# Optimization experiments

Measured on AMD Instinct MI355X. Metric: run time of the kernel, lower is better.

Reference implementation:

```python
import jax, jax.numpy as jnp
import numpy as np

INT_MIN = jnp.iinfo(jnp.int32).min


def setup_inputs() -> dict:
    key = jax.random.key(0)
    ks = jax.random.split(key, 12)
    N, E, H, R, T = 200000, 100000, 100, 172, 100
    return {
        'src': jax.random.randint(ks[0], (E,), 0, N, dtype=jnp.int32),
        'dst': jax.random.randint(ks[1], (E,), 0, N, dtype=jnp.int32),
        't': jax.random.randint(ks[2], (E,), 0, 1000000, dtype=jnp.int32),
        'raw_msg': jax.random.normal(ks[3], (E, R), dtype=jnp.float32),
        'memory': jax.random.normal(ks[4], (N, H), dtype=jnp.float32),
        'last_update': jax.random.randint(ks[5], (N,), 0, 1000, dtype=jnp.int32),
        'te_w': jax.random.normal(ks[6], (T, 1), dtype=jnp.float32) * 0.1,
        'te_b': jax.random.normal(ks[7], (T,), dtype=jnp.float32) * 0.1,
        'w_ih': jax.random.normal(ks[8], (3 * H, 2 * H + R + T), dtype=jnp.float32) * 0.05,
        'w_hh': jax.random.normal(ks[9], (3 * H, H), dtype=jnp.float32) * 0.05,
        'b_ih': jax.random.normal(ks[10], (3 * H,), dtype=jnp.float32) * 0.05,
        'b_hh': jax.random.normal(ks[11], (3 * H,), dtype=jnp.float32) * 0.05,
    }


def reference(src, dst, t, raw_msg, memory, last_update, te_w, te_b, w_ih, w_hh, b_ih, b_hh):
    N, H = memory.shape
    E = src.shape[0]

    def time_enc(t_rel):  # Linear(1, time_dim) then cos, t_rel: [E] float
        return jnp.cos(t_rel[:, None] * te_w[:, 0][None, :] + te_b[None, :])

    # IdentityMessage: concat(mem[src], mem[dst], raw_msg, t_enc); two streams (s and d)
    t_enc_s = time_enc((t - last_update[src]).astype(raw_msg.dtype))
    t_enc_d = time_enc((t - last_update[dst]).astype(raw_msg.dtype))
    msg_s = jnp.concatenate([memory[src], memory[dst], raw_msg, t_enc_s], axis=-1)
    msg_d = jnp.concatenate([memory[dst], memory[src], raw_msg, t_enc_d], axis=-1)

    msg = jnp.concatenate([msg_s, msg_d], axis=0)        # [2E, msg_dim]
    idx = jnp.concatenate([src, dst], axis=0)            # [2E]
    t2 = jnp.concatenate([t, t], axis=0)                 # [2E]

    # LastAggregator: per node pick the message with maximum timestamp
    max_t = jnp.full((N,), INT_MIN, dtype=t2.dtype).at[idx].max(t2)
    cand = jnp.where(t2 == max_t[idx], jnp.arange(2 * E, dtype=jnp.int32), jnp.int32(-1))
    win = jnp.full((N,), -1, dtype=jnp.int32).at[idx].max(cand)  # winning edge per node
    has_msg = win >= 0
    aggr = jnp.where(has_msg[:, None], msg[jnp.clip(win, 0)], 0.0)  # [N, msg_dim]

    # GRUCell(msg_dim, H)
    gi = aggr @ w_ih.T + b_ih                             # [N, 3H]
    gh = memory @ w_hh.T + b_hh                           # [N, 3H]
    i_r, i_z, i_n = jnp.split(gi, 3, axis=-1)
    h_r, h_z, h_n = jnp.split(gh, 3, axis=-1)
    r = jax.nn.sigmoid(i_r + h_r)
    z = jax.nn.sigmoid(i_z + h_z)
    n = jnp.tanh(i_n + r * h_n)
    memory_new = (1.0 - z) * n + z * memory               # [N, H]

    last_update_new = last_update.at[idx].max(t2)         # scatter latest event time
    return memory_new, last_update_new
```

## Files before the change

kernel.cpp:

```cpp
#include <hip/hip_runtime.h>
#include <math.h>

typedef __attribute__((ext_vector_type(8))) short  short8;
typedef __attribute__((ext_vector_type(4))) float  f32x4;

static constexpr int H     = 100;
static constexpr int RD    = 172;
static constexpr int WK    = 472;
static constexpr int NKS   = 20;
static constexpr int MB    = 48;
static constexpr int GRPS  = 3;
static constexpr int BLK   = 448;
static constexpr int SLOTS = 64;
static constexpr int NTT   = 28;
static constexpr int BPK_N = NTT * NKS * 64 * 8;

__device__ inline unsigned short f2bf(float x) {
    union { float f; unsigned u; } v; v.f = x;
    return (unsigned short)((v.u + 0x7FFFu + ((v.u >> 16) & 1u)) >> 16);
}
__device__ inline float bf2f(unsigned short b) {
    union { unsigned u; float f; } v; v.u = ((unsigned)b) << 16;
    return v.f;
}
__device__ inline unsigned pkbf(float a, float b) {
    unsigned r;
    asm("v_cvt_pk_bf16_f32 %0, %1, %2" : "=v"(r) : "v"(a), "v"(b));
    return r;
}
__device__ inline f32x4 mfma16(short8 a, short8 b, f32x4 c) {
    return __builtin_amdgcn_mfma_f32_16x16x32_bf16(a, b, c, 0, 0, 0);
}
__device__ inline float4 ld4g(const float* base, int lc, int limit) {
    if (lc + 4 <= limit) return *(const float4*)(base + lc);
    return make_float4(0.f, 0.f, 0.f, 0.f);
}

__global__ __launch_bounds__(256) void k_init(int* __restrict__ maxt, int* __restrict__ win, int N) {
    int i = blockIdx.x * blockDim.x + threadIdx.x;
    if (i < N) { maxt[i] = (int)0x80000000; win[i] = -1; }
}

__global__ __launch_bounds__(256) void k_maxt(const int* __restrict__ src, const int* __restrict__ dst,
                                              const int* __restrict__ t, int* __restrict__ maxt, int E) {
    int j = blockIdx.x * blockDim.x + threadIdx.x;
    if (j < E) {
        int tj = t[j];
        atomicMax(&maxt[src[j]], tj);
        atomicMax(&maxt[dst[j]], tj);
    }
}

__global__ __launch_bounds__(256) void k_win(const int* __restrict__ src, const int* __restrict__ dst,
                                             const int* __restrict__ t, const int* __restrict__ maxt,
                                             int* __restrict__ win, int E) {
    int j = blockIdx.x * blockDim.x + threadIdx.x;
    if (j < E) {
        int tj = t[j];
        int s = src[j], d = dst[j];
        if (maxt[s] == tj) atomicMax(&win[s], j);
        if (maxt[d] == tj) atomicMax(&win[d], j + E);
    }
}

__global__ __launch_bounds__(256) void k_prep(const float* __restrict__ w_ih, const float* __restrict__ w_hh,
                                              unsigned short* __restrict__ B) {
    int idx = blockIdx.x * 256 + threadIdx.x;
    if (idx >= BPK_N) return;
    int jj   = idx & 7;
    int lane = (idx >> 3) & 63;
    int rest = idx >> 9;
    int ks   = rest % NKS;
    int tile = rest / NKS;
    int kk   = ks * 32 + ((lane >> 4) << 3) + jj;
    float v = 0.f;
    if (tile < 21) {
        int gate = tile / 7;
        int tcol = (tile % 7) * 16 + (lane & 15);
        if (tcol < 100) {
            if (kk < 512) {
                int col = -1;
                if (kk < 100)                   col = kk;
                else if (kk >= 104 && kk < 204) col = kk - 4;
                else if (kk >= 208 && kk < 380) col = kk - 8;
                else if (kk >= 384 && kk < 484) col = kk - 12;
                if (col >= 0) v = w_ih[(gate * 100 + tcol) * WK + col];
            } else {
                int khh = kk - 512;
                if (gate < 2 && khh < 100)
                    v = w_hh[(gate * 100 + tcol) * H + khh];
            }
        }
    } else {
        int tcol = (tile - 21) * 16 + (lane & 15);
        int khh  = kk - 512;
        if (tcol < 100 && khh >= 0 && khh < 100)
            v = w_hh[(200 + tcol) * H + khh];
    }
    B[idx] = f2bf(v);
}

__global__ __launch_bounds__(BLK, 4) void k_gru(
    const int* __restrict__ src, const int* __restrict__ dst, const int* __restrict__ t,
    const float* __restrict__ raw_msg, const float* __restrict__ memory,
    const int* __restrict__ last_update, const float* __restrict__ te_w,
    const float* __restrict__ te_b, const float* __restrict__ b_ih,
    const float* __restrict__ b_hh, const int* __restrict__ win,
    const unsigned short* __restrict__ Bpack,
    float* __restrict__ out_mem, float* __restrict__ out_lu, int E, int N)
{
    __shared__ unsigned short sA[GRPS * NKS * SLOTS * 8];
    __shared__ int   s_other[MB];
    __shared__ int   s_j[MB];
    __shared__ int   s_has[MB];
    __shared__ float s_dt[MB];

    const int tid   = threadIdx.x;
    const int node0 = blockIdx.x * MB;

    if (tid < MB) {
        int node = node0 + tid;
        int has = 0, j = 0, other = 0; float dt = 0.f;
        if (node < N) {
            int lu = last_update[node];
            int w  = win[node];
            int te = lu;
            if (w >= 0) {
                has = 1;
                int e = (w < E) ? w : (w - E);
                j = e;
                other = (w < E) ? dst[e] : src[e];
                te = t[e];
                dt = (float)(te - lu);
            }
            out_lu[node] = (float)(te > lu ? te : lu);
        }
        s_j[tid] = j; s_other[tid] = other; s_has[tid] = has; s_dt[tid] = dt;
    }
    __syncthreads();

    if (tid < 432) {
        const int nl    = tid % 48;
        const int c0    = tid / 48;
        const int node  = node0 + nl;
        const bool valid = node < N;
        const int has   = s_has[nl];
        const float* memN = memory + (size_t)node * H;
        const float* memO = memory + (size_t)s_other[nl] * H;
        const float* rawJ = raw_msg + (size_t)s_j[nl] * RD;
        const float dt  = s_dt[nl];
        const int grp = nl >> 4;
        const int row = nl & 15;

        float4 va[8], vb[8];
#pragma unroll
        for (int it = 0; it < 8; ++it) {
            const int cc = c0 + it * 9;
            va[it] = make_float4(0.f, 0.f, 0.f, 0.f); vb[it] = va[it];
            if (cc < 67) {
                const int c  = cc + 13;
                const int kb = c * 8;
                if (c < 64) {
                    if (has) {
                        if (c < 26)      { va[it] = ld4g(memO, kb - 104, 100); vb[it] = ld4g(memO, kb - 100, 100); }
                        else if (c < 48) { va[it] = ld4g(rawJ, kb - 208, RD ); vb[it] = ld4g(rawJ, kb - 204, RD ); }
                        else {
                            const int lc = kb - 384;
                            float vv[8];
#pragma unroll
                            for (int q = 0; q < 8; ++q) {
                                int col = lc + q;
                                vv[q] = (col < 100) ? __cosf(fmaf(dt, te_w[col], te_b[col])) : 0.f;
                            }
                            va[it] = make_float4(vv[0], vv[1], vv[2], vv[3]);
                            vb[it] = make_float4(vv[4], vv[5], vv[6], vv[7]);
                        }
                    }
                } else if (valid) {
                    va[it] = ld4g(memN, kb - 512, 100);
                    vb[it] = ld4g(memN, kb - 508, 100);
                }
            }
        }
#pragma unroll
        for (int it = 0; it < 8; ++it) {
            const int cc = c0 + it * 9;
            if (cc < 67) {
                const int c = cc + 13;
                int4 sv;
                sv.x = (int)pkbf(va[it].x, va[it].y);
                sv.y = (int)pkbf(va[it].z, va[it].w);
                sv.z = (int)pkbf(vb[it].x, vb[it].y);
                sv.w = (int)pkbf(vb[it].z, vb[it].w);
                {
                    const int ks = c >> 2, sub = c & 3;
                    const int slot = sub * 16 + (row ^ (sub << 2));
                    *(int4*)&sA[((grp * NKS + ks) * SLOTS + slot) * 8] = sv;
                }
                if (c >= 64 && c < 77) {
                    int4 sm_;
                    sm_.x = has ? sv.x : 0; sm_.y = has ? sv.y : 0;
                    sm_.z = has ? sv.z : 0; sm_.w = has ? sv.w : 0;
                    const int cm = c - 64;
                    const int ks = cm >> 2, sub = cm & 3;
                    const int slot = sub * 16 + (row ^ (sub << 2));
                    *(int4*)&sA[((grp * NKS + ks) * SLOTS + slot) * 8] = sm_;
                }
            }
        }
    }
    __syncthreads();

    const int wv    = tid >> 6;
    const int lane  = tid & 63;
    const int lrow  = lane & 15;
    const int lhi   = lane >> 4;
    const int slotl = lhi * 16 + (lrow ^ (lhi << 2));

    f32x4 ar[GRPS], az[GRPS], an[GRPS], ah[GRPS];
#pragma unroll
    for (int m = 0; m < GRPS; ++m) { ar[m] = (f32x4)0.f; az[m] = (f32x4)0.f; an[m] = (f32x4)0.f; ah[m] = (f32x4)0.f; }

    __builtin_amdgcn_s_setprio(1);
#pragma unroll
    for (int ks = 0; ks < NKS; ++ks) {
        short8 a0 = *(const short8*)&sA[((0 * NKS + ks) * SLOTS + slotl) * 8];
        short8 a1 = *(const short8*)&sA[((1 * NKS + ks) * SLOTS + slotl) * 8];
        short8 a2 = *(const short8*)&sA[((2 * NKS + ks) * SLOTS + slotl) * 8];
        short8 br = *(const short8*)&Bpack[(((size_t)(     wv) * NKS + ks) * 64 + lane) * 8];
        short8 bz = *(const short8*)&Bpack[(((size_t)( 7 + wv) * NKS + ks) * 64 + lane) * 8];
        short8 bn = (ks < 16)
                  ? *(const short8*)&Bpack[(((size_t)(14 + wv) * NKS + ks) * 64 + lane) * 8]
                  : *(const short8*)&Bpack[(((size_t)(21 + wv) * NKS + ks) * 64 + lane) * 8];
        ar[0] = mfma16(a0, br, ar[0]);  ar[1] = mfma16(a1, br, ar[1]);  ar[2] = mfma16(a2, br, ar[2]);
        az[0] = mfma16(a0, bz, az[0]);  az[1] = mfma16(a1, bz, az[1]);  az[2] = mfma16(a2, bz, az[2]);
        if (ks < 16) { an[0] = mfma16(a0, bn, an[0]);  an[1] = mfma16(a1, bn, an[1]);  an[2] = mfma16(a2, bn, an[2]); }
        else         { ah[0] = mfma16(a0, bn, ah[0]);  ah[1] = mfma16(a1, bn, ah[1]);  ah[2] = mfma16(a2, bn, ah[2]); }
    }
    __builtin_amdgcn_s_setprio(0);

    const int c = wv * 16 + lrow;
    if (c < 100) {
        const float br_ = b_ih[c]       + b_hh[c];
        const float bz_ = b_ih[c + 100] + b_hh[c + 100];
        const float bin = b_ih[c + 200];
        const float bhn = b_hh[c + 200];
        const int ksh = 16 + (c >> 5);
        const int sbh = (c >> 3) & 3;
        const int ceh = c & 7;
#pragma unroll
        for (int m = 0; m < GRPS; ++m) {
#pragma unroll
            for (int r = 0; r < 4; ++r) {
                const int node = node0 + m * 16 + lhi * 4 + r;
                if (node < N) {
                    const int rw   = lhi * 4 + r;
                    const int slot = sbh * 16 + (rw ^ (sbh << 2));
                    const float h  = bf2f(sA[((m * NKS + ksh) * SLOTS + slot) * 8 + ceh]);
                    const float rg = 1.f / (1.f + __expf(-(ar[m][r] + br_)));
                    const float zg = 1.f / (1.f + __expf(-(az[m][r] + bz_)));
                    const float xn = an[m][r] + bin + rg * (ah[m][r] + bhn);
                    const float ex = __expf(2.f * fabsf(xn));
                    const float th = copysignf(1.f - 2.f / (ex + 1.f), xn);
                    out_mem[(size_t)node * H + c] = (1.f - zg) * th + zg * h;
                }
            }
        }
    }
}

extern "C" void kernel_launch(void* const* d_in, const int* in_sizes, int n_in,
                              void* d_out, int out_size, void* d_ws, size_t ws_size,
                              hipStream_t stream)
{
    const int*   src         = (const int*)d_in[0];
    const int*   dst         = (const int*)d_in[1];
    const int*   t           = (const int*)d_in[2];
    const float* raw_msg     = (const float*)d_in[3];
    const float* memory      = (const float*)d_in[4];
    const int*   last_update = (const int*)d_in[5];
    const float* te_w        = (const float*)d_in[6];
    const float* te_b        = (const float*)d_in[7];
    const float* w_ih        = (const float*)d_in[8];
    const float* w_hh        = (const float*)d_in[9];
    const float* b_ih        = (const float*)d_in[10];
    const float* b_hh        = (const float*)d_in[11];

    const int E = in_sizes[0];
    const int N = in_sizes[5];

    float* out    = (float*)d_out;
    float* out_lu = out + (size_t)N * H;

    int* maxt = (int*)d_ws;
    int* win  = maxt + N;
    unsigned short* Bpack = (unsigned short*)(win + N);

    k_init<<<(N + 255) / 256, 256, 0, stream>>>(maxt, win, N);
    k_prep<<<(BPK_N + 255) / 256, 256, 0, stream>>>(w_ih, w_hh, Bpack);
    k_maxt<<<(E + 255) / 256, 256, 0, stream>>>(src, dst, t, maxt, E);
    k_win <<<(E + 255) / 256, 256, 0, stream>>>(src, dst, t, maxt, win, E);
    k_gru <<<(N + MB - 1) / MB, BLK, 0, stream>>>(src, dst, t, raw_msg, memory, last_update,
                                                  te_w, te_b, b_ih, b_hh, win, Bpack,
                                                  out, out_lu, E, N);
}
```

Baseline: 188.5 us.

## Process four node tiles per block with double-buffered LDS staging

Each k_gru block now handles four 48-node tiles instead of one. The gathers for the next tile are issued into registers before the MFMA loop and epilogue of the current tile, then converted into the other half of a double-buffered LDS A buffer. The goal is to hide global gather latency behind matrix and epilogue work and to cut launch and per-block setup overhead. In exchange it doubles LDS use, raises register pressure because the va/vb registers stay live across the MFMA loop, lowers launch_bounds occupancy from 4 to 2, and launches four times fewer blocks.

```diff
diff --git a/kernel.cpp b/kernel.cpp
--- a/kernel.cpp
+++ b/kernel.cpp
@@ -12,6 +12,8 @@
 static constexpr int GRPS  = 3;
 static constexpr int BLK   = 448;
 static constexpr int SLOTS = 64;
+static constexpr int TPB   = 4;
+static constexpr int ABUF  = GRPS * NKS * SLOTS * 8;
 static constexpr int NTT   = 28;
 static constexpr int BPK_N = NTT * NKS * 64 * 8;
 
@@ -34,6 +36,13 @@
 __device__ inline float4 ld4g(const float* base, int lc, int limit) {
     if (lc + 4 <= limit) return *(const float4*)(base + lc);
     return make_float4(0.f, 0.f, 0.f, 0.f);
+}
+__device__ inline void pipe_barrier() {
+    __builtin_amdgcn_sched_barrier(0);
+    asm volatile("s_waitcnt lgkmcnt(0)" ::: "memory");
+    __builtin_amdgcn_sched_barrier(0);
+    __builtin_amdgcn_s_barrier();
+    __builtin_amdgcn_sched_barrier(0);
 }
 
 __global__ __launch_bounds__(256) void k_init(int* __restrict__ maxt, int* __restrict__ win, int N) {
@@ -100,7 +109,84 @@
     B[idx] = f2bf(v);
 }
 
-__global__ __launch_bounds__(BLK, 4) void k_gru(
+__device__ inline void issue_loads(int lt, int tid, int node_base, int N,
+                                   const int* s_j, const int* s_other, const int* s_has,
+                                   const float* memory, const float* raw_msg,
+                                   float4 (&va)[8], float4 (&vb)[8])
+{
+    if (tid >= 432) return;
+    const int nl = tid % 48, c0 = tid / 48;
+    const int node  = node_base + nl;
+    const bool valid = node < N;
+    const int has   = s_has[lt * MB + nl];
+    const float* memN = memory + (size_t)node * H;
+    const float* memO = memory + (size_t)s_other[lt * MB + nl] * H;
+    const float* rawJ = raw_msg + (size_t)s_j[lt * MB + nl] * RD;
+#pragma unroll
+    for (int it = 0; it < 8; ++it) {
+        const int cc = c0 + it * 9;
+        va[it] = make_float4(0.f, 0.f, 0.f, 0.f); vb[it] = va[it];
+        if (cc < 67) {
+            const int c = cc + 13, kb = c * 8;
+            if (c < 26)      { if (has)  { va[it] = ld4g(memO, kb - 104, 100); vb[it] = ld4g(memO, kb - 100, 100); } }
+            else if (c < 48) { if (has)  { va[it] = ld4g(rawJ, kb - 208, RD ); vb[it] = ld4g(rawJ, kb - 204, RD ); } }
+            else if (c < 64) {  }
+            else             { if (valid){ va[it] = ld4g(memN, kb - 512, 100); vb[it] = ld4g(memN, kb - 508, 100); } }
+        }
+    }
+}
+
+__device__ inline void cvt_write(int lt, int tid, unsigned short* __restrict__ buf,
+                                 const int* s_has, const float* s_dt,
+                                 const float* te_w, const float* te_b,
+                                 float4 (&va)[8], float4 (&vb)[8])
+{
+    if (tid >= 432) return;
+    const int nl = tid % 48, c0 = tid / 48;
+    const int has = s_has[lt * MB + nl];
+    const float dt = s_dt[lt * MB + nl];
+    const int grp = nl >> 4, row = nl & 15;
+#pragma unroll
+    for (int it = 0; it < 8; ++it) {
+        const int cc = c0 + it * 9;
+        if (cc >= 67) continue;
+        const int c = cc + 13;
+        if (c >= 48 && c < 64) {
+            if (has) {
+                const int lc = c * 8 - 384;
+                float vv[8];
+#pragma unroll
+                for (int q = 0; q < 8; ++q) {
+                    int col = lc + q;
+                    vv[q] = (col < 100) ? __cosf(fmaf(dt, te_w[col], te_b[col])) : 0.f;
+                }
+                va[it] = make_float4(vv[0], vv[1], vv[2], vv[3]);
+                vb[it] = make_float4(vv[4], vv[5], vv[6], vv[7]);
+            }
+        }
+        int4 sv;
+        sv.x = (int)pkbf(va[it].x, va[it].y);
+        sv.y = (int)pkbf(va[it].z, va[it].w);
+        sv.z = (int)pkbf(vb[it].x, vb[it].y);
+        sv.w = (int)pkbf(vb[it].z, vb[it].w);
+        {
+            const int ks = c >> 2, sub = c & 3;
+            const int slot = sub * 16 + (row ^ (sub << 2));
+            *(int4*)&buf[((grp * NKS + ks) * SLOTS + slot) * 8] = sv;
+        }
+        if (c >= 64 && c < 77) {
+            int4 sm_;
+            sm_.x = has ? sv.x : 0; sm_.y = has ? sv.y : 0;
+            sm_.z = has ? sv.z : 0; sm_.w = has ? sv.w : 0;
+            const int cm = c - 64;
+            const int ks = cm >> 2, sub = cm & 3;
+            const int slot = sub * 16 + (row ^ (sub << 2));
+            *(int4*)&buf[((grp * NKS + ks) * SLOTS + slot) * 8] = sm_;
+        }
+    }
+}
+
+__global__ __launch_bounds__(BLK, 2) void k_gru(
     const int* __restrict__ src, const int* __restrict__ dst, const int* __restrict__ t,
     const float* __restrict__ raw_msg, const float* __restrict__ memory,
     const int* __restrict__ last_update, const float* __restrict__ te_w,
@@ -109,17 +195,21 @@
     const unsigned short* __restrict__ Bpack,
     float* __restrict__ out_mem, float* __restrict__ out_lu, int E, int N)
 {
-    __shared__ unsigned short sA[GRPS * NKS * SLOTS * 8];
-    __shared__ int   s_other[MB];
-    __shared__ int   s_j[MB];
-    __shared__ int   s_has[MB];
-    __shared__ float s_dt[MB];
-
-    const int tid   = threadIdx.x;
-    const int node0 = blockIdx.x * MB;
-
-    if (tid < MB) {
-        int node = node0 + tid;
+    __shared__ unsigned short sA[2 * ABUF];
+    __shared__ int   s_other[TPB * MB];
+    __shared__ int   s_j[TPB * MB];
+    __shared__ int   s_has[TPB * MB];
+    __shared__ float s_dt[TPB * MB];
+
+    const int tid = threadIdx.x;
+    const int ntiles    = (N + MB - 1) / MB;
+    const int tile_base = blockIdx.x * TPB;
+    const int ntl       = min(TPB, ntiles - tile_base);
+    if (ntl <= 0) return;
+
+    for (int it0 = tid; it0 < ntl * MB; it0 += BLK) {
+        const int lt = it0 / MB, nl = it0 - lt * MB;
+        const int node = (tile_base + lt) * MB + nl;
         int has = 0, j = 0, other = 0; float dt = 0.f;
         if (node < N) {
             int lu = last_update[node];
@@ -135,79 +225,7 @@
             }
             out_lu[node] = (float)(te > lu ? te : lu);
         }
-        s_j[tid] = j; s_other[tid] = other; s_has[tid] = has; s_dt[tid] = dt;
-    }
-    __syncthreads();
-
-    if (tid < 432) {
-        const int nl    = tid % 48;
-        const int c0    = tid / 48;
-        const int node  = node0 + nl;
-        const bool valid = node < N;
-        const int has   = s_has[nl];
-        const float* memN = memory + (size_t)node * H;
-        const float* memO = memory + (size_t)s_other[nl] * H;
-        const float* rawJ = raw_msg + (size_t)s_j[nl] * RD;
-        const float dt  = s_dt[nl];
-        const int grp = nl >> 4;
-        const int row = nl & 15;
-
-        float4 va[8], vb[8];
-#pragma unroll
-        for (int it = 0; it < 8; ++it) {
-            const int cc = c0 + it * 9;
-            va[it] = make_float4(0.f, 0.f, 0.f, 0.f); vb[it] = va[it];
-            if (cc < 67) {
-                const int c  = cc + 13;
-                const int kb = c * 8;
-                if (c < 64) {
-                    if (has) {
-                        if (c < 26)      { va[it] = ld4g(memO, kb - 104, 100); vb[it] = ld4g(memO, kb - 100, 100); }
-                        else if (c < 48) { va[it] = ld4g(rawJ, kb - 208, RD ); vb[it] = ld4g(rawJ, kb - 204, RD ); }
-                        else {
-                            const int lc = kb - 384;
-                            float vv[8];
-#pragma unroll
-                            for (int q = 0; q < 8; ++q) {
-                                int col = lc + q;
-                                vv[q] = (col < 100) ? __cosf(fmaf(dt, te_w[col], te_b[col])) : 0.f;
-                            }
-                            va[it] = make_float4(vv[0], vv[1], vv[2], vv[3]);
-                            vb[it] = make_float4(vv[4], vv[5], vv[6], vv[7]);
-                        }
-                    }
-                } else if (valid) {
-                    va[it] = ld4g(memN, kb - 512, 100);
-                    vb[it] = ld4g(memN, kb - 508, 100);
-                }
-            }
-        }
-#pragma unroll
-        for (int it = 0; it < 8; ++it) {
-            const int cc = c0 + it * 9;
-            if (cc < 67) {
-                const int c = cc + 13;
-                int4 sv;
-                sv.x = (int)pkbf(va[it].x, va[it].y);
-                sv.y = (int)pkbf(va[it].z, va[it].w);
-                sv.z = (int)pkbf(vb[it].x, vb[it].y);
-                sv.w = (int)pkbf(vb[it].z, vb[it].w);
-                {
-                    const int ks = c >> 2, sub = c & 3;
-                    const int slot = sub * 16 + (row ^ (sub << 2));
-                    *(int4*)&sA[((grp * NKS + ks) * SLOTS + slot) * 8] = sv;
-                }
-                if (c >= 64 && c < 77) {
-                    int4 sm_;
-                    sm_.x = has ? sv.x : 0; sm_.y = has ? sv.y : 0;
-                    sm_.z = has ? sv.z : 0; sm_.w = has ? sv.w : 0;
-                    const int cm = c - 64;
-                    const int ks = cm >> 2, sub = cm & 3;
-                    const int slot = sub * 16 + (row ^ (sub << 2));
-                    *(int4*)&sA[((grp * NKS + ks) * SLOTS + slot) * 8] = sm_;
-                }
-            }
-        }
+        s_j[it0] = j; s_other[it0] = other; s_has[it0] = has; s_dt[it0] = dt;
     }
     __syncthreads();
 
@@ -217,55 +235,78 @@
     const int lhi   = lane >> 4;
     const int slotl = lhi * 16 + (lrow ^ (lhi << 2));
 
-    f32x4 ar[GRPS], az[GRPS], an[GRPS], ah[GRPS];
-#pragma unroll
-    for (int m = 0; m < GRPS; ++m) { ar[m] = (f32x4)0.f; az[m] = (f32x4)0.f; an[m] = (f32x4)0.f; ah[m] = (f32x4)0.f; }
-
-    __builtin_amdgcn_s_setprio(1);
-#pragma unroll
-    for (int ks = 0; ks < NKS; ++ks) {
-        short8 a0 = *(const short8*)&sA[((0 * NKS + ks) * SLOTS + slotl) * 8];
-        short8 a1 = *(const short8*)&sA[((1 * NKS + ks) * SLOTS + slotl) * 8];
-        short8 a2 = *(const short8*)&sA[((2 * NKS + ks) * SLOTS + slotl) * 8];
-        short8 br = *(const short8*)&Bpack[(((size_t)(     wv) * NKS + ks) * 64 + lane) * 8];
-        short8 bz = *(const short8*)&Bpack[(((size_t)( 7 + wv) * NKS + ks) * 64 + lane) * 8];
-        short8 bn = (ks < 16)
-                  ? *(const short8*)&Bpack[(((size_t)(14 + wv) * NKS + ks) * 64 + lane) * 8]
-                  : *(const short8*)&Bpack[(((size_t)(21 + wv) * NKS + ks) * 64 + lane) * 8];
-        ar[0] = mfma16(a0, br, ar[0]);  ar[1] = mfma16(a1, br, ar[1]);  ar[2] = mfma16(a2, br, ar[2]);
-        az[0] = mfma16(a0, bz, az[0]);  az[1] = mfma16(a1, bz, az[1]);  az[2] = mfma16(a2, bz, az[2]);
-        if (ks < 16) { an[0] = mfma16(a0, bn, an[0]);  an[1] = mfma16(a1, bn, an[1]);  an[2] = mfma16(a2, bn, an[2]); }
-        else         { ah[0] = mfma16(a0, bn, ah[0]);  ah[1] = mfma16(a1, bn, ah[1]);  ah[2] = mfma16(a2, bn, ah[2]); }
-    }
-    __builtin_amdgcn_s_setprio(0);
-
-    const int c = wv * 16 + lrow;
-    if (c < 100) {
-        const float br_ = b_ih[c]       + b_hh[c];
-        const float bz_ = b_ih[c + 100] + b_hh[c + 100];
-        const float bin = b_ih[c + 200];
-        const float bhn = b_hh[c + 200];
-        const int ksh = 16 + (c >> 5);
-        const int sbh = (c >> 3) & 3;
-        const int ceh = c & 7;
-#pragma unroll
-        for (int m = 0; m < GRPS; ++m) {
-#pragma unroll
-            for (int r = 0; r < 4; ++r) {
-                const int node = node0 + m * 16 + lhi * 4 + r;
-                if (node < N) {
-                    const int rw   = lhi * 4 + r;
-                    const int slot = sbh * 16 + (rw ^ (sbh << 2));
-                    const float h  = bf2f(sA[((m * NKS + ksh) * SLOTS + slot) * 8 + ceh]);
-                    const float rg = 1.f / (1.f + __expf(-(ar[m][r] + br_)));
-                    const float zg = 1.f / (1.f + __expf(-(az[m][r] + bz_)));
-                    const float xn = an[m][r] + bin + rg * (ah[m][r] + bhn);
-                    const float ex = __expf(2.f * fabsf(xn));
-                    const float th = copysignf(1.f - 2.f / (ex + 1.f), xn);
-                    out_mem[(size_t)node * H + c] = (1.f - zg) * th + zg * h;
+    float4 va[8], vb[8];
+
+    issue_loads(0, tid, tile_base * MB, N, s_j, s_other, s_has, memory, raw_msg, va, vb);
+    cvt_write(0, tid, sA, s_has, s_dt, te_w, te_b, va, vb);
+    pipe_barrier();
+
+    for (int i = 0; i < ntl; ++i) {
+        unsigned short* bufc = sA + (size_t)(i & 1) * ABUF;
+        unsigned short* bufn = sA + (size_t)((i + 1) & 1) * ABUF;
+
+        if (i + 1 < ntl)
+            issue_loads(i + 1, tid, (tile_base + i + 1) * MB, N, s_j, s_other, s_has,
+                        memory, raw_msg, va, vb);
+        __builtin_amdgcn_sched_barrier(0);
+
+        f32x4 ar[GRPS], az[GRPS], an[GRPS], ah[GRPS];
+#pragma unroll
+        for (int m = 0; m < GRPS; ++m) { ar[m] = (f32x4)0.f; az[m] = (f32x4)0.f; an[m] = (f32x4)0.f; ah[m] = (f32x4)0.f; }
+
+        __builtin_amdgcn_s_setprio(1);
+#pragma unroll
+        for (int ks = 0; ks < NKS; ++ks) {
+            short8 a0 = *(const short8*)&bufc[((0 * NKS + ks) * SLOTS + slotl) * 8];
+            short8 a1 = *(const short8*)&bufc[((1 * NKS + ks) * SLOTS + slotl) * 8];
+            short8 a2 = *(const short8*)&bufc[((2 * NKS + ks) * SLOTS + slotl) * 8];
+            short8 br = *(const short8*)&Bpack[(((size_t)(     wv) * NKS + ks) * 64 + lane) * 8];
+            short8 bz = *(const short8*)&Bpack[(((size_t)( 7 + wv) * NKS + ks) * 64 + lane) * 8];
+            short8 bn = (ks < 16)
+                      ? *(const short8*)&Bpack[(((size_t)(14 + wv) * NKS + ks) * 64 + lane) * 8]
+                      : *(const short8*)&Bpack[(((size_t)(21 + wv) * NKS + ks) * 64 + lane) * 8];
+            ar[0] = mfma16(a0, br, ar[0]);  ar[1] = mfma16(a1, br, ar[1]);  ar[2] = mfma16(a2, br, ar[2]);
+            az[0] = mfma16(a0, bz, az[0]);  az[1] = mfma16(a1, bz, az[1]);  az[2] = mfma16(a2, bz, az[2]);
+            if (ks < 16) { an[0] = mfma16(a0, bn, an[0]);  an[1] = mfma16(a1, bn, an[1]);  an[2] = mfma16(a2, bn, an[2]); }
+            else         { ah[0] = mfma16(a0, bn, ah[0]);  ah[1] = mfma16(a1, bn, ah[1]);  ah[2] = mfma16(a2, bn, ah[2]); }
+        }
+        __builtin_amdgcn_s_setprio(0);
+
+        {
+            const int node0 = (tile_base + i) * MB;
+            const int c = wv * 16 + lrow;
+            if (c < 100) {
+                const float br_ = b_ih[c]       + b_hh[c];
+                const float bz_ = b_ih[c + 100] + b_hh[c + 100];
+                const float bin = b_ih[c + 200];
+                const float bhn = b_hh[c + 200];
+                const int ksh = 16 + (c >> 5);
+                const int sbh = (c >> 3) & 3;
+                const int ceh = c & 7;
+#pragma unroll
+                for (int m = 0; m < GRPS; ++m) {
+#pragma unroll
+                    for (int r = 0; r < 4; ++r) {
+                        const int node = node0 + m * 16 + lhi * 4 + r;
+                        if (node < N) {
+                            const int rw   = lhi * 4 + r;
+                            const int slot = sbh * 16 + (rw ^ (sbh << 2));
+                            const float h  = bf2f(bufc[((m * NKS + ksh) * SLOTS + slot) * 8 + ceh]);
+                            const float rg = 1.f / (1.f + __expf(-(ar[m][r] + br_)));
+                            const float zg = 1.f / (1.f + __expf(-(az[m][r] + bz_)));
+                            const float xn = an[m][r] + bin + rg * (ah[m][r] + bhn);
+                            const float ex = __expf(2.f * fabsf(xn));
+                            const float th = copysignf(1.f - 2.f / (ex + 1.f), xn);
+                            out_mem[(size_t)node * H + c] = (1.f - zg) * th + zg * h;
+                        }
+                    }
                 }
             }
         }
+
+        if (i + 1 < ntl)
+            cvt_write(i + 1, tid, bufn, s_has, s_dt, te_w, te_b, va, vb);
+        pipe_barrier();
     }
 }
 
@@ -296,11 +337,14 @@
     int* win  = maxt + N;
     unsigned short* Bpack = (unsigned short*)(win + N);
 
+    const int ntiles = (N + MB - 1) / MB;
+    const int nblk   = (ntiles + TPB - 1) / TPB;
+
     k_init<<<(N + 255) / 256, 256, 0, stream>>>(maxt, win, N);
     k_prep<<<(BPK_N + 255) / 256, 256, 0, stream>>>(w_ih, w_hh, Bpack);
     k_maxt<<<(E + 255) / 256, 256, 0, stream>>>(src, dst, t, maxt, E);
     k_win <<<(E + 255) / 256, 256, 0, stream>>>(src, dst, t, maxt, win, E);
-    k_gru <<<(N + MB - 1) / MB, BLK, 0, stream>>>(src, dst, t, raw_msg, memory, last_update,
-                                                  te_w, te_b, b_ih, b_hh, win, Bpack,
-                                                  out, out_lu, E, N);
-}
+    k_gru <<<nblk, BLK, 0, stream>>>(src, dst, t, raw_msg, memory, last_update,
+                                     te_w, te_b, b_ih, b_hh, win, Bpack,
+                                     out, out_lu, E, N);
+}
```

Result: slower. 713.4 us (+278.5%).

## Split fused GRU kernel into segmented gather and GEMM passes

Applied to the files above, without the earlier changes.

Adds a per-node metadata kernel that also writes last_update, then processes nodes in workspace-sized segments. Each segment runs a gather kernel that builds bf16-packed A tiles in global memory, followed by a GEMM+GRU kernel that loads those tiles into LDS. The aim is to decouple the irregular, latency-bound gathers from the MFMA work so each kernel can get better occupancy. The cost is writing and reading back a large packed A buffer through HBM plus extra launches. The fused fallback, used when the workspace is too small, also drops its LDS swizzle and moves the time-encoding cos work into the store loop.

```diff
diff --git a/kernel.cpp b/kernel.cpp
--- a/kernel.cpp
+++ b/kernel.cpp
@@ -8,12 +8,14 @@
 static constexpr int RD    = 172;
 static constexpr int WK    = 472;
 static constexpr int NKS   = 20;
+static constexpr int CH    = 80;
 static constexpr int MB    = 48;
 static constexpr int GRPS  = 3;
 static constexpr int BLK   = 448;
-static constexpr int SLOTS = 64;
 static constexpr int NTT   = 28;
 static constexpr int BPK_N = NTT * NKS * 64 * 8;
+static constexpr int SEGMAX = 48000;
+static constexpr int SEGMIN = 8352;
 
 __device__ inline unsigned short f2bf(float x) {
     union { float f; unsigned u; } v; v.f = x;
@@ -40,7 +42,6 @@
     int i = blockIdx.x * blockDim.x + threadIdx.x;
     if (i < N) { maxt[i] = (int)0x80000000; win[i] = -1; }
 }
-
 __global__ __launch_bounds__(256) void k_maxt(const int* __restrict__ src, const int* __restrict__ dst,
                                               const int* __restrict__ t, int* __restrict__ maxt, int E) {
     int j = blockIdx.x * blockDim.x + threadIdx.x;
@@ -50,7 +51,6 @@
         atomicMax(&maxt[dst[j]], tj);
     }
 }
-
 __global__ __launch_bounds__(256) void k_win(const int* __restrict__ src, const int* __restrict__ dst,
                                              const int* __restrict__ t, const int* __restrict__ maxt,
                                              int* __restrict__ win, int E) {
@@ -61,6 +61,26 @@
         if (maxt[s] == tj) atomicMax(&win[s], j);
         if (maxt[d] == tj) atomicMax(&win[d], j + E);
     }
+}
+__global__ __launch_bounds__(256) void k_meta(const int* __restrict__ src, const int* __restrict__ dst,
+                                              const int* __restrict__ t, const int* __restrict__ last_update,
+                                              const int* __restrict__ win, int4* __restrict__ meta,
+                                              float* __restrict__ out_lu, int E, int N) {
+    int i = blockIdx.x * blockDim.x + threadIdx.x;
+    if (i >= N) return;
+    int lu = last_update[i], w = win[i];
+    int j = 0, other = 0, has = 0, te = lu; float dt = 0.f;
+    if (w >= 0) {
+        has = 1;
+        int e = (w < E) ? w : (w - E);
+        j = e;
+        other = (w < E) ? dst[e] : src[e];
+        te = t[e];
+        dt = (float)(te - lu);
+    }
+    out_lu[i] = (float)(te > lu ? te : lu);
+    int4 m; m.x = j; m.y = other; m.z = has; m.w = __float_as_int(dt);
+    meta[i] = m;
 }
 
 __global__ __launch_bounds__(256) void k_prep(const float* __restrict__ w_ih, const float* __restrict__ w_hh,
@@ -100,7 +120,137 @@
     B[idx] = f2bf(v);
 }
 
-__global__ __launch_bounds__(BLK, 4) void k_gru(
+__global__ __launch_bounds__(256) void k_gather(
+    const float* __restrict__ raw_msg, const float* __restrict__ memory,
+    const float* __restrict__ te_w, const float* __restrict__ te_b,
+    const int4* __restrict__ meta, unsigned short* __restrict__ Apack,
+    int node_base, int nthreads, int N)
+{
+    int id = blockIdx.x * 256 + threadIdx.x;
+    if (id >= nthreads) return;
+    const int row = id & 15;
+    const int cc  = id >> 4;
+    const int c   = cc % CH;
+    const int t16 = cc / CH;
+    const int node = node_base + t16 * 16 + row;
+    const bool vnode = node < N;
+
+    float4 va = make_float4(0.f, 0.f, 0.f, 0.f), vb = va;
+    int4 m = vnode ? meta[node] : make_int4(0, 0, 0, 0);
+    const int has = m.z;
+    const float dt = __int_as_float(m.w);
+
+    if (c < 13) {
+        if (has) { const float* p = memory + (size_t)node * H; int o = c * 8;
+                   va = ld4g(p, o, 100); vb = ld4g(p, o + 4, 100); }
+    } else if (c < 26) {
+        if (has) { const float* p = memory + (size_t)m.y * H; int o = (c - 13) * 8;
+                   va = ld4g(p, o, 100); vb = ld4g(p, o + 4, 100); }
+    } else if (c < 48) {
+        if (has) { const float* p = raw_msg + (size_t)m.x * RD; int o = (c - 26) * 8;
+                   va = ld4g(p, o, RD); vb = ld4g(p, o + 4, RD); }
+    } else if (c < 64) {
+        if (has) {
+            int o = (c - 48) * 8;
+            float4 w0 = ld4g(te_w, o, 100), w1 = ld4g(te_w, o + 4, 100);
+            float4 b0 = ld4g(te_b, o, 100), b1 = ld4g(te_b, o + 4, 100);
+            va.x = __cosf(fmaf(dt, w0.x, b0.x)); va.y = __cosf(fmaf(dt, w0.y, b0.y));
+            va.z = __cosf(fmaf(dt, w0.z, b0.z)); va.w = __cosf(fmaf(dt, w0.w, b0.w));
+            vb.x = __cosf(fmaf(dt, w1.x, b1.x)); vb.y = __cosf(fmaf(dt, w1.y, b1.y));
+            vb.z = __cosf(fmaf(dt, w1.z, b1.z)); vb.w = __cosf(fmaf(dt, w1.w, b1.w));
+        }
+    } else {
+        if (vnode) { const float* p = memory + (size_t)node * H; int o = (c - 64) * 8;
+                     va = ld4g(p, o, 100); vb = ld4g(p, o + 4, 100); }
+    }
+    int4 sv;
+    sv.x = (int)pkbf(va.x, va.y);
+    sv.y = (int)pkbf(va.z, va.w);
+    sv.z = (int)pkbf(vb.x, vb.y);
+    sv.w = (int)pkbf(vb.z, vb.w);
+    *(int4*)&Apack[(size_t)id * 8] = sv;
+}
+
+__global__ __launch_bounds__(BLK) void k_gemm(
+    const unsigned short* __restrict__ Apack, const unsigned short* __restrict__ Bpack,
+    const float* __restrict__ b_ih, const float* __restrict__ b_hh,
+    float* __restrict__ out_mem, int node_base, int N)
+{
+    __shared__ unsigned short sA[GRPS * NKS * 64 * 8];
+
+    const int tid  = threadIdx.x;
+    const int wv   = tid >> 6;
+    const int lane = tid & 63;
+    const int lrow = lane & 15;
+    const int lhi  = lane >> 4;
+    const int node0 = node_base + blockIdx.x * MB;
+    const size_t ab = (size_t)blockIdx.x * 60 * 512;
+
+    int4 x[9];
+#pragma unroll
+    for (int i = 0; i < 9; ++i) {
+        const int tl = wv + 7 * i;
+        if (tl < 60) x[i] = *(const int4*)&Apack[ab + (size_t)tl * 512 + lane * 8];
+    }
+#pragma unroll
+    for (int i = 0; i < 9; ++i) {
+        const int tl = wv + 7 * i;
+        if (tl < 60) *(int4*)&sA[tl * 512 + lane * 8] = x[i];
+    }
+    __syncthreads();
+
+    f32x4 ar[GRPS], az[GRPS], an[GRPS], ah[GRPS];
+#pragma unroll
+    for (int m = 0; m < GRPS; ++m) { ar[m] = (f32x4)0.f; az[m] = (f32x4)0.f; an[m] = (f32x4)0.f; ah[m] = (f32x4)0.f; }
+
+    __builtin_amdgcn_s_setprio(1);
+#pragma unroll
+    for (int ks = 0; ks < NKS; ++ks) {
+        short8 a0 = *(const short8*)&sA[(0 * NKS + ks) * 512 + lane * 8];
+        short8 a1 = *(const short8*)&sA[(1 * NKS + ks) * 512 + lane * 8];
+        short8 a2 = *(const short8*)&sA[(2 * NKS + ks) * 512 + lane * 8];
+        short8 br = *(const short8*)&Bpack[(((size_t)(     wv) * NKS + ks) * 64 + lane) * 8];
+        short8 bz = *(const short8*)&Bpack[(((size_t)( 7 + wv) * NKS + ks) * 64 + lane) * 8];
+        short8 bn = (ks < 16)
+                  ? *(const short8*)&Bpack[(((size_t)(14 + wv) * NKS + ks) * 64 + lane) * 8]
+                  : *(const short8*)&Bpack[(((size_t)(21 + wv) * NKS + ks) * 64 + lane) * 8];
+        ar[0] = mfma16(a0, br, ar[0]);  ar[1] = mfma16(a1, br, ar[1]);  ar[2] = mfma16(a2, br, ar[2]);
+        az[0] = mfma16(a0, bz, az[0]);  az[1] = mfma16(a1, bz, az[1]);  az[2] = mfma16(a2, bz, az[2]);
+        if (ks < 16) { an[0] = mfma16(a0, bn, an[0]);  an[1] = mfma16(a1, bn, an[1]);  an[2] = mfma16(a2, bn, an[2]); }
+        else         { ah[0] = mfma16(a0, bn, ah[0]);  ah[1] = mfma16(a1, bn, ah[1]);  ah[2] = mfma16(a2, bn, ah[2]); }
+    }
+    __builtin_amdgcn_s_setprio(0);
+
+    const int c = wv * 16 + lrow;
+    if (c < 100) {
+        const float br_ = b_ih[c]       + b_hh[c];
+        const float bz_ = b_ih[c + 100] + b_hh[c + 100];
+        const float bin = b_ih[c + 200];
+        const float bhn = b_hh[c + 200];
+        const int ksh = 16 + (c >> 5);
+        const int qh  = (c >> 3) & 3;
+        const int e   = c & 7;
+#pragma unroll
+        for (int m = 0; m < GRPS; ++m) {
+#pragma unroll
+            for (int r = 0; r < 4; ++r) {
+                const int node = node0 + m * 16 + lhi * 4 + r;
+                if (node < N) {
+                    const int rw = lhi * 4 + r;
+                    const float h  = bf2f(sA[(m * NKS + ksh) * 512 + (qh * 16 + rw) * 8 + e]);
+                    const float rg = 1.f / (1.f + __expf(-(ar[m][r] + br_)));
+                    const float zg = 1.f / (1.f + __expf(-(az[m][r] + bz_)));
+                    const float xn = an[m][r] + bin + rg * (ah[m][r] + bhn);
+                    const float ex = __expf(2.f * fabsf(xn));
+                    const float th = copysignf(1.f - 2.f / (ex + 1.f), xn);
+                    out_mem[(size_t)node * H + c] = (1.f - zg) * th + zg * h;
+                }
+            }
+        }
+    }
+}
+
+__global__ __launch_bounds__(BLK, 4) void k_gru_fused(
     const int* __restrict__ src, const int* __restrict__ dst, const int* __restrict__ t,
     const float* __restrict__ raw_msg, const float* __restrict__ memory,
     const int* __restrict__ last_update, const float* __restrict__ te_w,
@@ -109,7 +259,7 @@
     const unsigned short* __restrict__ Bpack,
     float* __restrict__ out_mem, float* __restrict__ out_lu, int E, int N)
 {
-    __shared__ unsigned short sA[GRPS * NKS * SLOTS * 8];
+    __shared__ unsigned short sA[GRPS * NKS * 64 * 8];
     __shared__ int   s_other[MB];
     __shared__ int   s_j[MB];
     __shared__ int   s_has[MB];
@@ -158,28 +308,11 @@
             const int cc = c0 + it * 9;
             va[it] = make_float4(0.f, 0.f, 0.f, 0.f); vb[it] = va[it];
             if (cc < 67) {
-                const int c  = cc + 13;
-                const int kb = c * 8;
-                if (c < 64) {
-                    if (has) {
-                        if (c < 26)      { va[it] = ld4g(memO, kb - 104, 100); vb[it] = ld4g(memO, kb - 100, 100); }
-                        else if (c < 48) { va[it] = ld4g(rawJ, kb - 208, RD ); vb[it] = ld4g(rawJ, kb - 204, RD ); }
-                        else {
-                            const int lc = kb - 384;
-                            float vv[8];
-#pragma unroll
-                            for (int q = 0; q < 8; ++q) {
-                                int col = lc + q;
-                                vv[q] = (col < 100) ? __cosf(fmaf(dt, te_w[col], te_b[col])) : 0.f;
-                            }
-                            va[it] = make_float4(vv[0], vv[1], vv[2], vv[3]);
-                            vb[it] = make_float4(vv[4], vv[5], vv[6], vv[7]);
-                        }
-                    }
-                } else if (valid) {
-                    va[it] = ld4g(memN, kb - 512, 100);
-                    vb[it] = ld4g(memN, kb - 508, 100);
-                }
+                const int c = cc + 13, kb = c * 8;
+                if (c < 26)      { if (has)  { va[it] = ld4g(memO, kb - 104, 100); vb[it] = ld4g(memO, kb - 100, 100); } }
+                else if (c < 48) { if (has)  { va[it] = ld4g(rawJ, kb - 208, RD ); vb[it] = ld4g(rawJ, kb - 204, RD ); } }
+                else if (c < 64) { }
+                else             { if (valid){ va[it] = ld4g(memN, kb - 512, 100); vb[it] = ld4g(memN, kb - 508, 100); } }
             }
         }
 #pragma unroll
@@ -187,6 +320,17 @@
             const int cc = c0 + it * 9;
             if (cc < 67) {
                 const int c = cc + 13;
+                if (c >= 48 && c < 64 && has) {
+                    const int lc = c * 8 - 384;
+                    float vv[8];
+#pragma unroll
+                    for (int q = 0; q < 8; ++q) {
+                        int col = lc + q;
+                        vv[q] = (col < 100) ? __cosf(fmaf(dt, te_w[col], te_b[col])) : 0.f;
+                    }
+                    va[it] = make_float4(vv[0], vv[1], vv[2], vv[3]);
+                    vb[it] = make_float4(vv[4], vv[5], vv[6], vv[7]);
+                }
                 int4 sv;
                 sv.x = (int)pkbf(va[it].x, va[it].y);
                 sv.y = (int)pkbf(va[it].z, va[it].w);
@@ -194,8 +338,7 @@
                 sv.w = (int)pkbf(vb[it].z, vb[it].w);
                 {
                     const int ks = c >> 2, sub = c & 3;
-                    const int slot = sub * 16 + (row ^ (sub << 2));
-                    *(int4*)&sA[((grp * NKS + ks) * SLOTS + slot) * 8] = sv;
+                    *(int4*)&sA[((grp * NKS + ks) * 64 + sub * 16 + row) * 8] = sv;
                 }
                 if (c >= 64 && c < 77) {
                     int4 sm_;
@@ -203,19 +346,17 @@
                     sm_.z = has ? sv.z : 0; sm_.w = has ? sv.w : 0;
                     const int cm = c - 64;
                     const int ks = cm >> 2, sub = cm & 3;
-                    const int slot = sub * 16 + (row ^ (sub << 2));
-                    *(int4*)&sA[((grp * NKS + ks) * SLOTS + slot) * 8] = sm_;
+                    *(int4*)&sA[((grp * NKS + ks) * 64 + sub * 16 + row) * 8] = sm_;
                 }
             }
         }
     }
     __syncthreads();
 
-    const int wv    = tid >> 6;
-    const int lane  = tid & 63;
-    const int lrow  = lane & 15;
-    const int lhi   = lane >> 4;
-    const int slotl = lhi * 16 + (lrow ^ (lhi << 2));
+    const int wv   = tid >> 6;
+    const int lane = tid & 63;
+    const int lrow = lane & 15;
+    const int lhi  = lane >> 4;
 
     f32x4 ar[GRPS], az[GRPS], an[GRPS], ah[GRPS];
 #pragma unroll
@@ -224,9 +365,9 @@
     __builtin_amdgcn_s_setprio(1);
 #pragma unroll
     for (int ks = 0; ks < NKS; ++ks) {
-        short8 a0 = *(const short8*)&sA[((0 * NKS + ks) * SLOTS + slotl) * 8];
-        short8 a1 = *(const short8*)&sA[((1 * NKS + ks) * SLOTS + slotl) * 8];
-        short8 a2 = *(const short8*)&sA[((2 * NKS + ks) * SLOTS + slotl) * 8];
+        short8 a0 = *(const short8*)&sA[(0 * NKS + ks) * 512 + lane * 8];
+        short8 a1 = *(const short8*)&sA[(1 * NKS + ks) * 512 + lane * 8];
+        short8 a2 = *(const short8*)&sA[(2 * NKS + ks) * 512 + lane * 8];
         short8 br = *(const short8*)&Bpack[(((size_t)(     wv) * NKS + ks) * 64 + lane) * 8];
         short8 bz = *(const short8*)&Bpack[(((size_t)( 7 + wv) * NKS + ks) * 64 + lane) * 8];
         short8 bn = (ks < 16)
@@ -246,17 +387,16 @@
         const float bin = b_ih[c + 200];
         const float bhn = b_hh[c + 200];
         const int ksh = 16 + (c >> 5);
-        const int sbh = (c >> 3) & 3;
-        const int ceh = c & 7;
+        const int qh  = (c >> 3) & 3;
+        const int e   = c & 7;
 #pragma unroll
         for (int m = 0; m < GRPS; ++m) {
 #pragma unroll
             for (int r = 0; r < 4; ++r) {
                 const int node = node0 + m * 16 + lhi * 4 + r;
                 if (node < N) {
-                    const int rw   = lhi * 4 + r;
-                    const int slot = sbh * 16 + (rw ^ (sbh << 2));
-                    const float h  = bf2f(sA[((m * NKS + ksh) * SLOTS + slot) * 8 + ceh]);
+                    const int rw = lhi * 4 + r;
+                    const float h  = bf2f(sA[(m * NKS + ksh) * 512 + (qh * 16 + rw) * 8 + e]);
                     const float rg = 1.f / (1.f + __expf(-(ar[m][r] + br_)));
                     const float zg = 1.f / (1.f + __expf(-(az[m][r] + bz_)));
                     const float xn = an[m][r] + bin + rg * (ah[m][r] + bhn);
@@ -292,15 +432,38 @@
     float* out    = (float*)d_out;
     float* out_lu = out + (size_t)N * H;
 
-    int* maxt = (int*)d_ws;
+    char* ws = (char*)d_ws;
+    int* maxt = (int*)ws;
     int* win  = maxt + N;
     unsigned short* Bpack = (unsigned short*)(win + N);
+    int4* meta = (int4*)(Bpack + BPK_N);
+    unsigned short* Apack = (unsigned short*)((char*)(meta + N));
+
+    const size_t aux = (size_t)N * 8 + (size_t)BPK_N * 2 + (size_t)N * 16;
+    long segN = 0;
+    if (ws_size > aux + 4096) segN = (long)((ws_size - aux - 4096) / (CH * 16));
+    segN = (segN / MB) * MB;
+    if (segN > SEGMAX) segN = SEGMAX;
 
     k_init<<<(N + 255) / 256, 256, 0, stream>>>(maxt, win, N);
     k_prep<<<(BPK_N + 255) / 256, 256, 0, stream>>>(w_ih, w_hh, Bpack);
     k_maxt<<<(E + 255) / 256, 256, 0, stream>>>(src, dst, t, maxt, E);
     k_win <<<(E + 255) / 256, 256, 0, stream>>>(src, dst, t, maxt, win, E);
-    k_gru <<<(N + MB - 1) / MB, BLK, 0, stream>>>(src, dst, t, raw_msg, memory, last_update,
-                                                  te_w, te_b, b_ih, b_hh, win, Bpack,
-                                                  out, out_lu, E, N);
-}
+
+    if (segN >= SEGMIN) {
+        k_meta<<<(N + 255) / 256, 256, 0, stream>>>(src, dst, t, last_update, win, meta, out_lu, E, N);
+        const long Npad = ((long)N + MB - 1) / MB * MB;
+        for (long base = 0; base < Npad; base += segN) {
+            const long nodes_s = (Npad - base < segN) ? (Npad - base) : segN;
+            const int  gth     = (int)(nodes_s * CH);
+            k_gather<<<(gth + 255) / 256, 256, 0, stream>>>(raw_msg, memory, te_w, te_b,
+                                                            meta, Apack, (int)base, gth, N);
+            k_gemm<<<(int)(nodes_s / MB), BLK, 0, stream>>>(Apack, Bpack, b_ih, b_hh,
+                                                            out, (int)base, N);
+        }
+    } else {
+        k_gru_fused<<<(N + MB - 1) / MB, BLK, 0, stream>>>(src, dst, t, raw_msg, memory, last_update,
+                                                           te_w, te_b, b_ih, b_hh, win, Bpack,
+                                                           out, out_lu, E, N);
+    }
+}
```

Result: slower. 354.9 us (+88.3%).
